# Performance work log

Hardware: AMD Instinct MI355X
Metric: run time of the kernel (lower is better)

Reference implementation:

```python
import jax, jax.numpy as jnp
import numpy as np

BS = 15
NA = BS * BS
NOISE_SCALE = 2.0
TEMP = 0.03
VALUE_NOISE = 200.0

def _build_windows():
    # all length-5 windows in the 4 directions of a 15x15 board (572 total)
    wins = []
    for dr, dc in ((0, 1), (1, 0), (1, 1), (1, -1)):
        for r in range(BS):
            for c in range(BS):
                er, ec = r + 4 * dr, c + 4 * dc
                if 0 <= er < BS and 0 <= ec < BS:
                    wins.append([(r + k * dr) * BS + (c + k * dc) for k in range(5)])
    return np.asarray(wins, dtype=np.int32)

_WIN = _build_windows()                      # [572, 5] flat cell indices
_NW = _WIN.shape[0]
_Mnp = np.zeros((NA, _NW), dtype=np.float32)  # membership: cell i in window w
for w in range(_NW):
    _Mnp[_WIN[w], w] = 1.0
WIN_CELLS = jnp.asarray(_WIN)
MEMBER = jnp.asarray(_Mnp)                   # [225, 572]
WEIGHTS = jnp.asarray([0.0, 5.0, 50.0, 500.0, 5000.0, 100000.0], dtype=jnp.float32)

def _window_score(pc, oc):
    # matches _eval_board's per-window scoring table
    sp = jnp.where((oc == 0) & (pc > 0), WEIGHTS[jnp.minimum(pc, 5)], 0.0)
    so = jnp.where((pc == 0) & (oc > 0), WEIGHTS[jnp.minimum(oc, 5)], 0.0)
    return sp - so

def setup_inputs() -> dict:
    key = jax.random.key(0)
    k1, k2, k3, k4 = jax.random.split(key, 4)
    B = 8192
    boards = jax.random.randint(k1, (B, NA), 0, 3, dtype=jnp.int32)
    current_player = jax.random.randint(k2, (B,), 1, 3, dtype=jnp.int32)
    policy_noise = jax.random.normal(k3, (B, NA), dtype=jnp.float32)
    value_noise = jax.random.normal(k4, (B,), dtype=jnp.float32)
    return {"boards": boards, "current_player": current_player,
            "policy_noise": policy_noise, "value_noise": value_noise}

def reference(boards, current_player, policy_noise, value_noise):
    player = current_player[:, None, None]           # [B,1,1]
    opp = 3 - player
    cells = boards[:, WIN_CELLS]                      # [B, 572, 5]
    pc0 = jnp.sum(cells == player, axis=-1)           # [B, 572] player stones per window
    oc0 = jnp.sum(cells == opp, axis=-1)              # [B, 572] opponent stones per window
    s0 = _window_score(pc0, oc0)                      # base per-window score
    base = jnp.sum(s0, axis=-1)                       # [B] = _eval_board(board, player)
    # placing a player stone in an empty cell adds +1 to pc of every window containing it
    d = _window_score(pc0 + 1, oc0) - s0              # [B, 572]
    delta = jnp.einsum('bw,aw->ba', d, MEMBER)        # [B, 225]
    win_w = ((pc0 == 4) & (oc0 == 0)).astype(jnp.float32)
    win = jnp.einsum('bw,aw->ba', win_w, MEMBER) > 0  # [B, 225]
    empty = boards == 0
    logits = jnp.where(empty, jnp.where(win, 1e5, base[:, None] + delta), -1e6)
    valid = logits > -1e5                             # matches `logits > -100000.0`
    n = jnp.sum(valid, axis=-1).astype(jnp.float32)
    nsafe = jnp.maximum(n, 1.0)
    mean = jnp.sum(jnp.where(valid, logits, 0.0), axis=-1) / nsafe
    var = jnp.sum(jnp.where(valid, (logits - mean[:, None]) ** 2, 0.0), axis=-1) / nsafe
    std = jnp.maximum(1.0, jnp.sqrt(var))             # population std, floored at 1
    logits = logits + jnp.where(valid & (n[:, None] > 0),
                                policy_noise * NOISE_SCALE * std[:, None], 0.0)
    policy = jax.nn.softmax(logits * TEMP, axis=-1)   # [B, 225]
    value = jnp.clip(jnp.tanh((base + value_noise * VALUE_NOISE) / 3000.0), -0.95, 0.95)[:, None]
    return policy, value
```

## Files before the change

### kernel.cpp

```cpp
#include <hip/hip_runtime.h>
#include <math.h>

#define BSZ 15
#define NA  225
#define NW  572

__device__ __forceinline__ float wtab(int n) {
    return n == 1 ? 5.f : n == 2 ? 50.f : n == 3 ? 500.f : n == 4 ? 5000.f : 100000.f;
}
__device__ __forceinline__ float wscore(int pc, int oc) {
    if (oc == 0 && pc > 0) return wtab(pc);
    if (pc == 0 && oc > 0) return -wtab(oc);
    return 0.f;
}

__device__ __forceinline__ float wredSum(float v) {
    #pragma unroll
    for (int off = 32; off; off >>= 1) v += __shfl_xor(v, off, 64);
    return v;
}
__device__ __forceinline__ float wredMax(float v) {
    #pragma unroll
    for (int off = 32; off; off >>= 1) v = fmaxf(v, __shfl_xor(v, off, 64));
    return v;
}

__global__ __launch_bounds__(256, 8) void heur_kernel(
    const int* __restrict__ boards, const int* __restrict__ cur,
    const float* __restrict__ pnoise, const float* __restrict__ vnoise,
    float* __restrict__ out, int B)
{
    const int wid  = threadIdx.x >> 6;
    const int lane = threadIdx.x & 63;
    const int b    = blockIdx.x * 4 + wid;

    __shared__ int   sB[4][NA];
    __shared__ float sDelta[4][NA];
    __shared__ float sWin[4][NA];

    if (b >= B) return;

    int*   __restrict__ bB = sB[wid];
    float* __restrict__ bD = sDelta[wid];
    float* __restrict__ bW = sWin[wid];

    const int player = cur[b];
    const int opp    = 3 - player;
    const int* __restrict__ gb = boards + (size_t)b * NA;

    #pragma unroll
    for (int j = 0; j < 4; ++j) {
        const int c = lane + 64 * j;
        if (c < NA) { bB[c] = gb[c]; bD[c] = 0.f; bW[c] = 0.f; }
    }
    __threadfence_block();

    float baseLocal = 0.f;
    #pragma unroll
    for (int it = 0; it < 9; ++it) {
        const int w = lane + it * 64;
        if (w < NW) {
            int r, c, step;
            if (w < 165)      {                  r = w / 11; c = w % 11;     step = 1;  }
            else if (w < 330) { const int u = w - 165; r = u / 15; c = u % 15;     step = 15; }
            else if (w < 451) { const int u = w - 330; r = u / 11; c = u % 11;     step = 16; }
            else              { const int u = w - 451; r = u / 11; c = u % 11 + 4; step = 14; }
            const int idx = r * BSZ + c;

            int pc = 0, oc = 0;
            #pragma unroll
            for (int k = 0; k < 5; ++k) {
                const int v = bB[idx + k * step];
                pc += (v == player);
                oc += (v == opp);
            }
            const float s0 = wscore(pc, oc);
            baseLocal += s0;
            const float d = wscore(pc + 1, oc) - s0;
            if (d != 0.f) {
                #pragma unroll
                for (int k = 0; k < 5; ++k) atomicAdd(&bD[idx + k * step], d);
            }
            if (pc == 4 && oc == 0) {
                #pragma unroll
                for (int k = 0; k < 5; ++k) bW[idx + k * step] = 1.f;
            }
        }
    }
    __threadfence_block();

    const float base = wredSum(baseLocal);

    float logitv[4];
    float nLoc = 0.f, sLoc = 0.f;
    #pragma unroll
    for (int j = 0; j < 4; ++j) {
        const int c = lane + 64 * j;
        float lg = -1000000.f;
        if (c < NA) {
            if (bB[c] == 0) lg = (bW[c] > 0.f) ? 100000.f : base + bD[c];
        }
        logitv[j] = lg;
        if (c < NA && lg > -100000.f) { nLoc += 1.f; sLoc += lg; }
    }
    #pragma unroll
    for (int off = 32; off; off >>= 1) {
        nLoc += __shfl_xor(nLoc, off, 64);
        sLoc += __shfl_xor(sLoc, off, 64);
    }
    const float nsafe = fmaxf(nLoc, 1.f);
    const float mean  = sLoc / nsafe;

    float vLoc = 0.f;
    #pragma unroll
    for (int j = 0; j < 4; ++j) {
        const int c = lane + 64 * j;
        if (c < NA && logitv[j] > -100000.f) {
            const float dv = logitv[j] - mean;
            vLoc += dv * dv;
        }
    }
    const float var  = wredSum(vLoc) / nsafe;
    const float std_ = fmaxf(1.f, sqrtf(var));
    const float nsc  = 2.0f * std_;
    const bool  anyValid = nLoc > 0.f;

    const float* __restrict__ pn = pnoise + (size_t)b * NA;
    #pragma unroll
    for (int j = 0; j < 4; ++j) {
        const int c = lane + 64 * j;
        if (c < NA && logitv[j] > -100000.f && anyValid)
            logitv[j] += pn[c] * nsc;
    }

    float xs[4];
    float mLoc = -INFINITY;
    #pragma unroll
    for (int j = 0; j < 4; ++j) {
        const int c = lane + 64 * j;
        xs[j] = logitv[j] * 0.03f;
        if (c < NA) mLoc = fmaxf(mLoc, xs[j]);
    }
    const float m = wredMax(mLoc);

    float ev[4];
    float eLoc = 0.f;
    #pragma unroll
    for (int j = 0; j < 4; ++j) {
        const int c = lane + 64 * j;
        ev[j] = (c < NA) ? __expf(xs[j] - m) : 0.f;
        eLoc += ev[j];
    }
    const float inv = 1.f / wredSum(eLoc);

    float* __restrict__ po = out + (size_t)b * NA;
    #pragma unroll
    for (int j = 0; j < 4; ++j) {
        const int c = lane + 64 * j;
        if (c < NA) po[c] = ev[j] * inv;
    }

    if (lane == 0) {
        float v = tanhf((base + vnoise[b] * 200.0f) / 3000.0f);
        v = fminf(0.95f, fmaxf(-0.95f, v));
        out[(size_t)B * NA + b] = v;
    }
}

extern "C" void kernel_launch(void* const* d_in, const int* in_sizes, int n_in,
                              void* d_out, int out_size, void* d_ws, size_t ws_size,
                              hipStream_t stream) {
    const int*   boards = (const int*)d_in[0];
    const int*   cur    = (const int*)d_in[1];
    const float* pn     = (const float*)d_in[2];
    const float* vn     = (const float*)d_in[3];
    float*       outp   = (float*)d_out;
    const int B = in_sizes[1];

    const int grid = (B + 3) / 4;
    heur_kernel<<<grid, 256, 0, stream>>>(boards, cur, pn, vn, outp, B);
}
```

Baseline: 111.5 us.

## Count window stones with wave ballot bitboards instead of shared-memory board reads

```diff
diff --git a/kernel.cpp b/kernel.cpp
--- a/kernel.cpp
+++ b/kernel.cpp
@@ -3,7 +3,7 @@
 
 #define BSZ 15
 #define NA  225
-#define NW  572
+typedef unsigned long long u64;
 
 __device__ __forceinline__ float wtab(int n) {
     return n == 1 ? 5.f : n == 2 ? 50.f : n == 3 ? 500.f : n == 4 ? 5000.f : 100000.f;
@@ -13,7 +13,6 @@
     if (pc == 0 && oc > 0) return -wtab(oc);
     return 0.f;
 }
-
 __device__ __forceinline__ float wredSum(float v) {
     #pragma unroll
     for (int off = 32; off; off >>= 1) v += __shfl_xor(v, off, 64);
@@ -23,6 +22,42 @@
     #pragma unroll
     for (int off = 32; off; off >>= 1) v = fmaxf(v, __shfl_xor(v, off, 64));
     return v;
+}
+
+struct Masks { u64 P0, P1, P2, P3, O0, O1, O2, O3; };
+
+template<int STEP, int DIV, int CEXTRA, bool HAS64>
+__device__ __forceinline__ void doWin(int u, const Masks& M, u64 wmask,
+                                      float* __restrict__ bD, float* __restrict__ bW,
+                                      float& baseLocal)
+{
+    const int r   = u / DIV;
+    const int c   = u % DIV + CEXTRA;
+    const int idx = r * BSZ + c;
+    const int q = idx >> 6, sh = idx & 63;
+    const u64 Plo = (q & 2) ? ((q & 1) ? M.P3 : M.P2) : ((q & 1) ? M.P1 : M.P0);
+    const u64 Phi = (q & 2) ? ((q & 1) ? 0ULL : M.P3) : ((q & 1) ? M.P2 : M.P1);
+    const u64 Olo = (q & 2) ? ((q & 1) ? M.O3 : M.O2) : ((q & 1) ? M.O1 : M.O0);
+    const u64 Ohi = (q & 2) ? ((q & 1) ? 0ULL : M.O3) : ((q & 1) ? M.O2 : M.O1);
+    const u64 xP = (Plo >> sh) | ((Phi << (63 - sh)) << 1);
+    const u64 xO = (Olo >> sh) | ((Ohi << (63 - sh)) << 1);
+    int pc = __popcll(xP & wmask);
+    int oc = __popcll(xO & wmask);
+    if (HAS64) {
+        pc += (int)((Phi >> sh) & 1ULL);
+        oc += (int)((Ohi >> sh) & 1ULL);
+    }
+    const float s0 = wscore(pc, oc);
+    baseLocal += s0;
+    const float d = wscore(pc + 1, oc) - s0;
+    if (d != 0.f) {
+        #pragma unroll
+        for (int k = 0; k < 5; ++k) atomicAdd(&bD[idx + k * STEP], d);
+    }
+    if (pc == 4 && oc == 0) {
+        #pragma unroll
+        for (int k = 0; k < 5; ++k) bW[idx + k * STEP] = 1.f;
+    }
 }
 
 __global__ __launch_bounds__(256, 8) void heur_kernel(
@@ -34,13 +69,11 @@
     const int lane = threadIdx.x & 63;
     const int b    = blockIdx.x * 4 + wid;
 
-    __shared__ int   sB[4][NA];
     __shared__ float sDelta[4][NA];
     __shared__ float sWin[4][NA];
 
     if (b >= B) return;
 
-    int*   __restrict__ bB = sB[wid];
     float* __restrict__ bD = sDelta[wid];
     float* __restrict__ bW = sWin[wid];
 
@@ -48,48 +81,52 @@
     const int opp    = 3 - player;
     const int* __restrict__ gb = boards + (size_t)b * NA;
 
-    #pragma unroll
-    for (int j = 0; j < 4; ++j) {
-        const int c = lane + 64 * j;
-        if (c < NA) { bB[c] = gb[c]; bD[c] = 0.f; bW[c] = 0.f; }
-    }
+    const int v0 = gb[lane];
+    const int v1 = gb[lane + 64];
+    const int v2 = gb[lane + 128];
+    const int v3 = (lane + 192 < NA) ? gb[lane + 192] : -1;
+
+    const float* __restrict__ pn = pnoise + (size_t)b * NA;
+    float pnv[4];
+    pnv[0] = pn[lane];
+    pnv[1] = pn[lane + 64];
+    pnv[2] = pn[lane + 128];
+    pnv[3] = (lane + 192 < NA) ? pn[lane + 192] : 0.f;
+    const float vnb = vnoise[b];
+
+    Masks M;
+    M.P0 = __ballot(v0 == player); M.O0 = __ballot(v0 == opp);
+    M.P1 = __ballot(v1 == player); M.O1 = __ballot(v1 == opp);
+    M.P2 = __ballot(v2 == player); M.O2 = __ballot(v2 == opp);
+    M.P3 = __ballot(v3 == player); M.O3 = __ballot(v3 == opp);
+
+    bD[lane] = 0.f;       bW[lane] = 0.f;
+    bD[lane + 64] = 0.f;  bW[lane + 64] = 0.f;
+    bD[lane + 128] = 0.f; bW[lane + 128] = 0.f;
+    if (lane + 192 < NA) { bD[lane + 192] = 0.f; bW[lane + 192] = 0.f; }
     __threadfence_block();
 
     float baseLocal = 0.f;
-    #pragma unroll
-    for (int it = 0; it < 9; ++it) {
-        const int w = lane + it * 64;
-        if (w < NW) {
-            int r, c, step;
-            if (w < 165)      {                  r = w / 11; c = w % 11;     step = 1;  }
-            else if (w < 330) { const int u = w - 165; r = u / 15; c = u % 15;     step = 15; }
-            else if (w < 451) { const int u = w - 330; r = u / 11; c = u % 11;     step = 16; }
-            else              { const int u = w - 451; r = u / 11; c = u % 11 + 4; step = 14; }
-            const int idx = r * BSZ + c;
-
-            int pc = 0, oc = 0;
-            #pragma unroll
-            for (int k = 0; k < 5; ++k) {
-                const int v = bB[idx + k * step];
-                pc += (v == player);
-                oc += (v == opp);
-            }
-            const float s0 = wscore(pc, oc);
-            baseLocal += s0;
-            const float d = wscore(pc + 1, oc) - s0;
-            if (d != 0.f) {
-                #pragma unroll
-                for (int k = 0; k < 5; ++k) atomicAdd(&bD[idx + k * step], d);
-            }
-            if (pc == 4 && oc == 0) {
-                #pragma unroll
-                for (int k = 0; k < 5; ++k) bW[idx + k * step] = 1.f;
-            }
-        }
-    }
+    doWin<1, 11, 0, false>(lane,       M, 0x1FULL, bD, bW, baseLocal);
+    doWin<1, 11, 0, false>(lane + 64,  M, 0x1FULL, bD, bW, baseLocal);
+    if (lane < 37)
+        doWin<1, 11, 0, false>(lane + 128, M, 0x1FULL, bD, bW, baseLocal);
+    doWin<15, 15, 0, false>(lane,      M, 0x1000200040008001ULL, bD, bW, baseLocal);
+    doWin<15, 15, 0, false>(lane + 64, M, 0x1000200040008001ULL, bD, bW, baseLocal);
+    if (lane < 37)
+        doWin<15, 15, 0, false>(lane + 128, M, 0x1000200040008001ULL, bD, bW, baseLocal);
+    doWin<16, 11, 0, true>(lane,       M, 0x0001000100010001ULL, bD, bW, baseLocal);
+    if (lane < 57)
+        doWin<16, 11, 0, true>(lane + 64, M, 0x0001000100010001ULL, bD, bW, baseLocal);
+    doWin<14, 11, 4, false>(lane,      M, 0x0100040010004001ULL, bD, bW, baseLocal);
+    if (lane < 57)
+        doWin<14, 11, 4, false>(lane + 64, M, 0x0100040010004001ULL, bD, bW, baseLocal);
+
     __threadfence_block();
 
     const float base = wredSum(baseLocal);
+
+    const u64 C0 = M.P0 | M.O0, C1 = M.P1 | M.O1, C2 = M.P2 | M.O2, C3 = M.P3 | M.O3;
 
     float logitv[4];
     float nLoc = 0.f, sLoc = 0.f;
@@ -98,7 +135,9 @@
         const int c = lane + 64 * j;
         float lg = -1000000.f;
         if (c < NA) {
-            if (bB[c] == 0) lg = (bW[c] > 0.f) ? 100000.f : base + bD[c];
+            const u64 Cj = j == 0 ? C0 : j == 1 ? C1 : j == 2 ? C2 : C3;
+            const bool isEmpty = ((Cj >> lane) & 1ULL) == 0ULL;
+            if (isEmpty) lg = (bW[c] > 0.f) ? 100000.f : base + bD[c];
         }
         logitv[j] = lg;
         if (c < NA && lg > -100000.f) { nLoc += 1.f; sLoc += lg; }
@@ -125,12 +164,11 @@
     const float nsc  = 2.0f * std_;
     const bool  anyValid = nLoc > 0.f;
 
-    const float* __restrict__ pn = pnoise + (size_t)b * NA;
     #pragma unroll
     for (int j = 0; j < 4; ++j) {
         const int c = lane + 64 * j;
         if (c < NA && logitv[j] > -100000.f && anyValid)
-            logitv[j] += pn[c] * nsc;
+            logitv[j] += pnv[j] * nsc;
     }
 
     float xs[4];
@@ -161,7 +199,7 @@
     }
 
     if (lane == 0) {
-        float v = tanhf((base + vnoise[b] * 200.0f) / 3000.0f);
+        float v = tanhf((base + vnb * 200.0f) / 3000.0f);
         v = fminf(0.95f, fmaxf(-0.95f, v));
         out[(size_t)B * NA + b] = v;
     }
```

Result: no change. 109.8 us (-1.5%).
